# Kernel tuning notes

Hardware: AMD Instinct MI355X
Metric: run time of the kernel (lower is better)

Reference implementation:

```python
import jax, jax.numpy as jnp
import numpy as np

NEG_SLOPE = 0.2  # PyG GATConv default leaky_relu negative slope

N_NODES = 10000
N_EDGES = 80000
IN_FEAT = 200
HID = 400
IN_HEADS = 8
OUT_FEAT = 200


def setup_inputs() -> dict:
    key = jax.random.key(0)
    ks = jax.random.split(key, 12)
    input_data = jax.random.normal(ks[0], (N_NODES, IN_FEAT), dtype=jnp.float32)
    edge_index = jax.random.randint(ks[1], (2, N_EDGES), 0, N_NODES, dtype=jnp.int64)
    # conv1: GATConv(200 -> 400, heads=8, concat=True)
    W1 = jax.random.normal(ks[2], (IN_FEAT, IN_HEADS * HID), dtype=jnp.float32) * 0.05
    a_src1 = jax.random.normal(ks[3], (IN_HEADS, HID), dtype=jnp.float32) * 0.05
    a_dst1 = jax.random.normal(ks[4], (IN_HEADS, HID), dtype=jnp.float32) * 0.05
    b1 = jnp.zeros((IN_HEADS * HID,), dtype=jnp.float32)
    # conv2: GATConv(3200 -> 200, heads=1, concat=False)
    W2 = jax.random.normal(ks[5], (IN_HEADS * HID, 1 * OUT_FEAT), dtype=jnp.float32) * 0.05
    a_src2 = jax.random.normal(ks[6], (1, OUT_FEAT), dtype=jnp.float32) * 0.05
    a_dst2 = jax.random.normal(ks[7], (1, OUT_FEAT), dtype=jnp.float32) * 0.05
    b2 = jnp.zeros((OUT_FEAT,), dtype=jnp.float32)
    return {"input_data": input_data, "edge_index": edge_index,
            "W1": W1, "a_src1": a_src1, "a_dst1": a_dst1, "b1": b1,
            "W2": W2, "a_src2": a_src2, "a_dst2": a_dst2, "b2": b2}


def _gat_conv(x, src, dst, W, a_src, a_dst, b, heads, out_ch, concat):
    """PyG GATConv (v1 attention), eval mode (no dropout)."""
    n = x.shape[0]
    h = (x @ W).reshape(n, heads, out_ch)              # [N,H,C]
    al_s = jnp.sum(h * a_src, axis=-1)                 # [N,H]
    al_d = jnp.sum(h * a_dst, axis=-1)                 # [N,H]
    e = jax.nn.leaky_relu(al_s[src] + al_d[dst], NEG_SLOPE)  # [E,H]
    # segment softmax over edges sharing the same destination node
    e_max = jax.ops.segment_max(e, dst, num_segments=n)       # [N,H]
    e_exp = jnp.exp(e - e_max[dst])                            # [E,H]
    denom = jax.ops.segment_sum(e_exp, dst, num_segments=n)   # [N,H]
    alpha = e_exp / denom[dst]                                 # [E,H]
    msg = h[src] * alpha[:, :, None]                           # [E,H,C]
    out = jax.ops.segment_sum(msg, dst, num_segments=n)       # [N,H,C]
    out = out.reshape(n, heads * out_ch) if concat else out.mean(axis=1)
    return out + b


def reference(input_data, edge_index, W1, a_src1, a_dst1, b1, W2, a_src2, a_dst2, b2):
    n = input_data.shape[0]
    loop = jnp.arange(n, dtype=edge_index.dtype)
    src = jnp.concatenate([edge_index[0], loop])  # add self-loops (PyG default)
    dst = jnp.concatenate([edge_index[1], loop])
    # eval mode: F.dropout is identity
    x = _gat_conv(input_data, src, dst, W1, a_src1, a_dst1, b1, IN_HEADS, HID, True)
    x = jax.nn.elu(x)
    x = _gat_conv(x, src, dst, W2, a_src2, a_dst2, b2, 1, OUT_FEAT, False)
    return x
```

## Files before the change

kernel.cpp:

```cpp
#include <hip/hip_runtime.h>
#include <math.h>

#define N_NODES 10000
#define N_EDGES 80000
#define ET (N_EDGES + N_NODES)
#define IN_FEAT 200
#define HID 400
#define NH1 8
#define F1 (NH1 * HID)
#define OUT_FEAT 200
#define NEG_SLOPE 0.2f

#define M_PAD 10048
#define K1 224
#define HSL (NH1 * K1)
#define XH_K 416
#define C1P 448
#define KALL (NH1 * XH_K)
#define N2P2 256
#define XHS 456
#define NQ 4

typedef __attribute__((ext_vector_type(8))) short short8_t;
typedef __attribute__((ext_vector_type(4))) float f32x4;


__device__ inline void edge_sd(const int* __restrict__ ei, int e, int& s, int& d) {
    if (e < N_EDGES) { s = ei[e]; d = ei[N_EDGES + e]; }
    else { s = e - N_EDGES; d = s; }
}

__device__ inline unsigned short f2bf(float x) {
    unsigned u = __float_as_uint(x);
    unsigned r = u + 0x7FFFu + ((u >> 16) & 1u);
    return (unsigned short)(r >> 16);
}

__device__ inline void sm_merge(float& m, float& l, float m2, float l2) {
    float mn = fmaxf(m, m2);
    float t1 = (m  > -1e30f) ? l  * __expf(m  - mn) : 0.f;
    float t2 = (m2 > -1e30f) ? l2 * __expf(m2 - mn) : 0.f;
    m = mn; l = t1 + t2;
}

#define W1N (NH1 * C1P * K1)
#define W2N (N2P2 * KALL)
__global__ __launch_bounds__(256) void prep_w(const float* __restrict__ W1,
                                              const float* __restrict__ W2,
                                              unsigned short* __restrict__ W1f,
                                              unsigned short* __restrict__ W2f) {
    int idx = blockIdx.x * blockDim.x + threadIdx.x;
    if (idx < W1N) {
        int e    = idx & 7;
        int lane = (idx >> 3) & 63;
        int rem  = idx >> 9;
        int ks   = rem % 7;
        int jgh  = rem / 7;
        int jg   = jgh % 28;
        int h    = jgh / 28;
        int c = jg * 16 + (lane & 15);
        int k = ks * 32 + (lane >> 4) * 8 + e;
        float v = (k < IN_FEAT && c < HID) ? W1[(size_t)k * F1 + h * HID + c] : 0.f;
        W1f[idx] = f2bf(v);
    } else if (idx < W1N + W2N) {
        int t    = idx - W1N;
        int e    = t & 7;
        int lane = (t >> 3) & 63;
        int rem  = t >> 9;
        int ks   = rem % 13;
        int cgh  = rem / 13;
        int cg   = cgh % 16;
        int h    = cgh / 16;
        int c = cg * 16 + (lane & 15);
        int k = ks * 32 + (lane >> 4) * 8 + e;
        float v = (c < OUT_FEAT && k < HID) ? W2[(size_t)(h * HID + k) * OUT_FEAT + c] : 0.f;
        W2f[t] = f2bf(v);
    }
}

__global__ __launch_bounds__(256) void pvec_k(const float* __restrict__ W1,
                                              const float* __restrict__ a_src,
                                              const float* __restrict__ a_dst,
                                              float* __restrict__ p_src,
                                              float* __restrict__ p_dst) {
    int idx = blockIdx.x * blockDim.x + threadIdx.x;
    if (idx >= 2 * NH1 * IN_FEAT) return;
    int which = idx / (NH1 * IN_FEAT);
    int r = idx - which * (NH1 * IN_FEAT);
    int h = r / IN_FEAT, k = r - h * IN_FEAT;
    const float* av = (which == 0 ? a_src : a_dst) + h * HID;
    const float* wrow = W1 + (size_t)k * F1 + h * HID;
    float acc = 0.f;
    for (int c = 0; c < HID; ++c) acc += wrow[c] * av[c];
    (which == 0 ? p_src : p_dst)[h * IN_FEAT + k] = acc;
}

__global__ __launch_bounds__(512) void att1x(const float* __restrict__ X,
                                             const float* __restrict__ p_src,
                                             const float* __restrict__ p_dst,
                                             float* __restrict__ als,
                                             float* __restrict__ ald) {
    const int n    = blockIdx.x;
    const int head = threadIdx.x >> 6;
    const int lane = threadIdx.x & 63;
    const float* xp = X + (size_t)n * IN_FEAT;
    const float* ps = p_src + head * IN_FEAT;
    const float* pd = p_dst + head * IN_FEAT;
    float ss = 0.f, sd = 0.f;
    for (int k = lane; k < IN_FEAT; k += 64) {
        float v = xp[k];
        ss += v * ps[k];
        sd += v * pd[k];
    }
    for (int off = 32; off; off >>= 1) {
        ss += __shfl_down(ss, off);
        sd += __shfl_down(sd, off);
    }
    if (lane == 0) { als[n * NH1 + head] = ss; ald[n * NH1 + head] = sd; }
}

__global__ __launch_bounds__(256) void count_k(const int* __restrict__ ei, int* __restrict__ counts) {
    int e = blockIdx.x * blockDim.x + threadIdx.x;
    if (e >= ET) return;
    int s, d; edge_sd(ei, e, s, d);
    atomicAdd(&counts[d], 1);
}

__global__ __launch_bounds__(1024) void scan_k(const int* __restrict__ counts, int* __restrict__ offs) {
    __shared__ int part[1024];
    const int tid = threadIdx.x;
    const int base = tid * 10;
    int loc[10];
    int s = 0;
    for (int i = 0; i < 10; ++i) {
        int idx = base + i;
        int c = (idx < N_NODES) ? counts[idx] : 0;
        loc[i] = s; s += c;
    }
    part[tid] = s;
    __syncthreads();
    for (int off = 1; off < 1024; off <<= 1) {
        int v = (tid >= off) ? part[tid - off] : 0;
        __syncthreads();
        part[tid] += v;
        __syncthreads();
    }
    int pre = (tid > 0) ? part[tid - 1] : 0;
    for (int i = 0; i < 10; ++i) {
        int idx = base + i;
        if (idx < N_NODES) offs[idx] = pre + loc[i];
    }
    if (tid == 1023) offs[N_NODES] = part[1023];
}

__global__ __launch_bounds__(256) void scatter_k(const int* __restrict__ ei,
                                                 const int* __restrict__ offs,
                                                 int* __restrict__ cursor,
                                                 int* __restrict__ esrc) {
    int e = blockIdx.x * blockDim.x + threadIdx.x;
    if (e >= ET) return;
    int s, d; edge_sd(ei, e, s, d);
    int pos = atomicAdd(&cursor[d], 1);
    esrc[offs[d] + pos] = s;
}

__global__ __launch_bounds__(512) void agg1x(const float* __restrict__ X,
                                             const float* __restrict__ als1,
                                             const float* __restrict__ ald1,
                                             const int* __restrict__ offs,
                                             const int* __restrict__ esrc,
                                             unsigned short* __restrict__ xaggb) {
    __shared__ unsigned short sb[8][HSL];
    const int wave = threadIdx.x >> 6;
    const int lane = threadIdx.x & 63;
    const int n = blockIdx.x * 8 + wave;

    if (n < N_NODES) {
        float acc[NH1][4];
#pragma unroll
        for (int h = 0; h < NH1; ++h)
#pragma unroll
            for (int g = 0; g < 4; ++g) acc[h][g] = 0.f;

        const int beg = offs[n], end = offs[n + 1];
        const int grp = lane >> 3;
        const int hd  = lane & 7;
        const float aldv = ald1[n * NH1 + hd];

        float m = -INFINITY, l = 0.f;
        for (int t = beg + grp; t < end; t += 8) {
            const int s = esrc[t];
            float v = als1[s * NH1 + hd] + aldv;
            v = v > 0.f ? v : NEG_SLOPE * v;
            float mn = fmaxf(m, v);
            l = l * __expf(m - mn) + __expf(v - mn);
            m = mn;
        }
#pragma unroll
        for (int off = 8; off < 64; off <<= 1) {
            float m2 = __shfl_xor(m, off);
            float l2 = __shfl_xor(l, off);
            sm_merge(m, l, m2, l2);
        }
        const float inv_l = 1.f / l;

        for (int t = beg; t < end; ++t) {
            const int s = esrc[t];
            float aval = 0.f;
            if (lane < NH1) {
                float v = als1[s * NH1 + lane] + aldv;
                v = v > 0.f ? v : NEG_SLOPE * v;
                aval = __expf(v - m) * inv_l;
            }
            const float* xp = X + (size_t)s * IN_FEAT;
            float x0 = xp[lane];
            float x1 = xp[64 + lane];
            float x2 = xp[128 + lane];
            float x3 = (lane < 8) ? xp[192 + lane] : 0.f;
#pragma unroll
            for (int h = 0; h < NH1; ++h) {
                float a = __shfl(aval, h);
                acc[h][0] += a * x0;
                acc[h][1] += a * x1;
                acc[h][2] += a * x2;
                acc[h][3] += a * x3;
            }
        }
#pragma unroll
        for (int h = 0; h < NH1; ++h) {
            sb[wave][h * K1 + lane]        = f2bf(acc[h][0]);
            sb[wave][h * K1 + 64 + lane]   = f2bf(acc[h][1]);
            sb[wave][h * K1 + 128 + lane]  = f2bf(acc[h][2]);
            if (lane < 32) {
                unsigned short v3 = (lane < 8) ? f2bf(acc[h][3]) : (unsigned short)0;
                sb[wave][h * K1 + 192 + lane] = v3;
            }
        }
    } else {
        for (int j = lane; j < HSL; j += 64) sb[wave][j] = 0;
    }
    __syncthreads();
    const uint4* s4 = (const uint4*)(&sb[0][0]);
    uint4* d4 = (uint4*)(xaggb + (size_t)blockIdx.x * 8 * HSL);
    for (int c = threadIdx.x; c < 8 * HSL / 8; c += 512) d4[c] = s4[c];
}

__global__ __launch_bounds__(512, 2) void fused_gemm(const unsigned short* __restrict__ xaggb,
                                                     const unsigned short* __restrict__ W1f,
                                                     const float* __restrict__ b1,
                                                     const unsigned short* __restrict__ W2f,
                                                     float* __restrict__ h2p) {
    __shared__ unsigned short xhf[32 * XHS];
    const int wave = threadIdx.x >> 6;
    const int lane = threadIdx.x & 63;
    const int row  = lane & 15;
    const int kg   = lane >> 4;
    const int rg   = wave & 1;
    const int cg   = wave >> 1;
    const int m0   = blockIdx.x * 32 + rg * 16;
    const int c0   = cg * 112;
    const int c2   = cg * 64;

    f32x4 oacc[4];
#pragma unroll
    for (int j = 0; j < 4; ++j) oacc[j] = (f32x4){0.f, 0.f, 0.f, 0.f};

#pragma unroll
    for (int hh = 0; hh < 2; ++hh) {
        const int h = blockIdx.y * 2 + hh;
        if (hh > 0) __syncthreads();

        const unsigned short* ap = xaggb + (size_t)(m0 + row) * HSL + h * K1 + kg * 8;
        short8_t areg[7];
#pragma unroll
        for (int ks = 0; ks < 7; ++ks)
            areg[ks] = *(const short8_t*)(ap + ks * 32);

        const unsigned short* w1h = W1f + (((size_t)h * 28 + cg * 7) * 7) * 512 + lane * 8;
        f32x4 acc[7];
#pragma unroll
        for (int j = 0; j < 7; ++j) acc[j] = (f32x4){0.f, 0.f, 0.f, 0.f};
#pragma unroll
        for (int ks = 0; ks < 7; ++ks) {
            short8_t b[7];
#pragma unroll
            for (int j = 0; j < 7; ++j)
                b[j] = *(const short8_t*)(w1h + (size_t)(j * 7 + ks) * 512);
#pragma unroll
            for (int j = 0; j < 7; ++j)
                acc[j] = __builtin_amdgcn_mfma_f32_16x16x32_bf16(areg[ks], b[j], acc[j], 0, 0, 0);
        }

#pragma unroll
        for (int j = 0; j < 7; ++j) {
            int cc = c0 + j * 16 + row;
            float bias = (cc < HID) ? b1[h * HID + cc] : 0.f;
#pragma unroll
            for (int r = 0; r < 4; ++r) {
                int rl = rg * 16 + kg * 4 + r;
                float v = acc[j][r] + bias;
                v = v > 0.f ? v : (__expf(v) - 1.f);
                xhf[rl * XHS + cc] = f2bf(v);
            }
        }
        __syncthreads();

        const unsigned short* w2h = W2f + (((size_t)h * 16 + cg * 4) * 13) * 512 + lane * 8;
        const int rl = rg * 16 + row;
#pragma unroll
        for (int ks = 0; ks < 13; ++ks) {
            short8_t b[4];
#pragma unroll
            for (int j = 0; j < 4; ++j)
                b[j] = *(const short8_t*)(w2h + (size_t)(j * 13 + ks) * 512);
            short8_t a = *(const short8_t*)&xhf[rl * XHS + ks * 32 + kg * 8];
#pragma unroll
            for (int j = 0; j < 4; ++j)
                oacc[j] = __builtin_amdgcn_mfma_f32_16x16x32_bf16(a, b[j], oacc[j], 0, 0, 0);
        }
    }

    float* op = h2p + ((size_t)blockIdx.y * M_PAD + (m0 + kg * 4)) * OUT_FEAT;
#pragma unroll
    for (int j = 0; j < 4; ++j) {
        int cc = c2 + j * 16 + row;
        if (cc < OUT_FEAT) {
#pragma unroll
            for (int r = 0; r < 4; ++r)
                op[(size_t)r * OUT_FEAT + cc] = oacc[j][r];
        }
    }
}

__global__ __launch_bounds__(256) void reduce_att2(const float* __restrict__ h2p,
                                                   const float* __restrict__ a_src,
                                                   const float* __restrict__ a_dst,
                                                   float* __restrict__ h2,
                                                   float* __restrict__ als,
                                                   float* __restrict__ ald) {
    const int wave = threadIdx.x >> 6;
    const int lane = threadIdx.x & 63;
    const int row  = blockIdx.x * 4 + wave;

    f32x4 sum = {0.f, 0.f, 0.f, 0.f};
    if (lane < 50) {
        const float* p = h2p + (size_t)row * OUT_FEAT + lane * 4;
#pragma unroll
        for (int q = 0; q < NQ; ++q)
            sum += *(const f32x4*)(p + (size_t)q * M_PAD * OUT_FEAT);
        *(f32x4*)(h2 + (size_t)row * OUT_FEAT + lane * 4) = sum;
    }
    float ss = 0.f, sd = 0.f;
    if (lane < 50) {
        f32x4 as = *(const f32x4*)(a_src + lane * 4);
        f32x4 ad = *(const f32x4*)(a_dst + lane * 4);
#pragma unroll
        for (int j = 0; j < 4; ++j) { ss += sum[j] * as[j]; sd += sum[j] * ad[j]; }
    }
    for (int off = 32; off; off >>= 1) {
        ss += __shfl_down(ss, off);
        sd += __shfl_down(sd, off);
    }
    if (lane == 0 && row < N_NODES) { als[row] = ss; ald[row] = sd; }
}

__global__ __launch_bounds__(256) void agg2_csr(const float* __restrict__ h2,
                                                const float* __restrict__ als2,
                                                const float* __restrict__ ald2,
                                                const int* __restrict__ offs,
                                                const int* __restrict__ esrc,
                                                const float* __restrict__ b2,
                                                float* __restrict__ out) {
    __shared__ float sm, sl;
    const int n = blockIdx.x;
    const int k = threadIdx.x;
    const float aldn = ald2[n];
    const int beg = offs[n], end = offs[n + 1];

    if (k < 64) {
        float m = -INFINITY, l = 0.f;
        for (int t = beg + k; t < end; t += 64) {
            int s = esrc[t];
            float v = als2[s] + aldn;
            v = v > 0.f ? v : NEG_SLOPE * v;
            float mn = fmaxf(m, v);
            l = l * __expf(m - mn) + __expf(v - mn);
            m = mn;
        }
#pragma unroll
        for (int off = 1; off < 64; off <<= 1) {
            float m2 = __shfl_xor(m, off);
            float l2 = __shfl_xor(l, off);
            sm_merge(m, l, m2, l2);
        }
        if (k == 0) { sm = m; sl = 1.f / l; }
    }
    __syncthreads();
    const float m = sm, inv_l = sl;

    if (k >= OUT_FEAT) return;
    float acc = 0.f;
    for (int t = beg; t < end; ++t) {
        int s = esrc[t];
        float v = als2[s] + aldn;
        v = v > 0.f ? v : NEG_SLOPE * v;
        float a = __expf(v - m) * inv_l;
        acc += a * h2[(size_t)s * OUT_FEAT + k];
    }
    out[(size_t)n * OUT_FEAT + k] = acc + b2[k];
}

extern "C" void kernel_launch(void* const* d_in, const int* in_sizes, int n_in,
                              void* d_out, int out_size, void* d_ws, size_t ws_size,
                              hipStream_t stream) {
    const float* X   = (const float*)d_in[0];
    const int*   ei  = (const int*)d_in[1];
    const float* W1  = (const float*)d_in[2];
    const float* as1 = (const float*)d_in[3];
    const float* ad1 = (const float*)d_in[4];
    const float* b1  = (const float*)d_in[5];
    const float* W2  = (const float*)d_in[6];
    const float* as2 = (const float*)d_in[7];
    const float* ad2 = (const float*)d_in[8];
    const float* b2  = (const float*)d_in[9];
    float* out = (float*)d_out;

    char* base = (char*)d_ws;
    auto carve = [&](size_t bytes) -> void* {
        void* p = (void*)base;
        base += (bytes + 255) & ~(size_t)255;
        return p;
    };
    float* p_src1 = (float*)carve(NH1 * IN_FEAT * 4);
    float* p_dst1 = (float*)carve(NH1 * IN_FEAT * 4);
    float* als1   = (float*)carve(N_NODES * NH1 * 4);
    float* ald1   = (float*)carve(N_NODES * NH1 * 4);
    float* als2   = (float*)carve(N_NODES * 4);
    float* ald2   = (float*)carve(N_NODES * 4);
    float* h2     = (float*)carve((size_t)M_PAD * OUT_FEAT * 4);
    int* counts   = (int*)carve(N_NODES * 4);
    int* cursor   = (int*)carve(N_NODES * 4);
    int* offs     = (int*)carve((N_NODES + 1) * 4);
    int* esrc     = (int*)carve(ET * 4);
    unsigned short* xaggb = (unsigned short*)carve((size_t)M_PAD * HSL * 2);
    unsigned short* W1f   = (unsigned short*)carve((size_t)W1N * 2);
    unsigned short* W2f   = (unsigned short*)carve((size_t)W2N * 2);
    float* h2p    = (float*)carve((size_t)NQ * M_PAD * OUT_FEAT * 4);

    hipMemsetAsync(counts, 0, 2 * 40192, stream);

    count_k<<<(ET + 255) / 256, 256, 0, stream>>>(ei, counts);
    scan_k<<<1, 1024, 0, stream>>>(counts, offs);
    scatter_k<<<(ET + 255) / 256, 256, 0, stream>>>(ei, offs, cursor, esrc);
    prep_w<<<(W1N + W2N + 255) / 256, 256, 0, stream>>>(W1, W2, W1f, W2f);
    pvec_k<<<(2 * NH1 * IN_FEAT + 255) / 256, 256, 0, stream>>>(W1, as1, ad1, p_src1, p_dst1);
    att1x<<<N_NODES, 512, 0, stream>>>(X, p_src1, p_dst1, als1, ald1);

    agg1x<<<M_PAD / 8, 512, 0, stream>>>(X, als1, ald1, offs, esrc, xaggb);

    fused_gemm<<<dim3(M_PAD / 32, NQ), 512, 0, stream>>>(xaggb, W1f, b1, W2f, h2p);

    reduce_att2<<<M_PAD / 4, 256, 0, stream>>>(h2p, as2, ad2, h2, als2, ald2);

    agg2_csr<<<N_NODES, 256, 0, stream>>>(h2, als2, ald2, offs, esrc, b2, out);
}
```

Baseline: 235.7 us.

## Merge preprocessing kernels and store aggregated features in MFMA fragment layout

Weight prep, edge counting and attention-vector projection now run as one launch, and the scatter runs together with the layer-1 attention logits in a second launch. This cuts the number of kernel launches and lets independent work overlap inside each launch. The aggregation kernel also writes its bf16 output directly in the 16-row MFMA A-fragment tile order, so the fused GEMM loads each fragment with contiguous per-lane reads instead of strided row reads. In exchange, the agg1x store becomes a scattered 16-byte write pattern, and the merged kernels run with block sizes that do not suit every branch.

Measured after the change: 218.7 us, median of 2. -7.2%, faster.

```diff
diff --git a/kernel.cpp b/kernel.cpp
--- a/kernel.cpp
+++ b/kernel.cpp
@@ -45,85 +45,67 @@
 
 #define W1N (NH1 * C1P * K1)
 #define W2N (N2P2 * KALL)
-__global__ __launch_bounds__(256) void prep_w(const float* __restrict__ W1,
-                                              const float* __restrict__ W2,
-                                              unsigned short* __restrict__ W1f,
-                                              unsigned short* __restrict__ W2f) {
-    int idx = blockIdx.x * blockDim.x + threadIdx.x;
-    if (idx < W1N) {
-        int e    = idx & 7;
-        int lane = (idx >> 3) & 63;
-        int rem  = idx >> 9;
-        int ks   = rem % 7;
-        int jgh  = rem / 7;
-        int jg   = jgh % 28;
-        int h    = jgh / 28;
-        int c = jg * 16 + (lane & 15);
-        int k = ks * 32 + (lane >> 4) * 8 + e;
-        float v = (k < IN_FEAT && c < HID) ? W1[(size_t)k * F1 + h * HID + c] : 0.f;
-        W1f[idx] = f2bf(v);
-    } else if (idx < W1N + W2N) {
-        int t    = idx - W1N;
-        int e    = t & 7;
-        int lane = (t >> 3) & 63;
-        int rem  = t >> 9;
-        int ks   = rem % 13;
-        int cgh  = rem / 13;
-        int cg   = cgh % 16;
-        int h    = cgh / 16;
-        int c = cg * 16 + (lane & 15);
-        int k = ks * 32 + (lane >> 4) * 8 + e;
-        float v = (c < OUT_FEAT && k < HID) ? W2[(size_t)(h * HID + k) * OUT_FEAT + c] : 0.f;
-        W2f[t] = f2bf(v);
-    }
-}
-
-__global__ __launch_bounds__(256) void pvec_k(const float* __restrict__ W1,
-                                              const float* __restrict__ a_src,
-                                              const float* __restrict__ a_dst,
-                                              float* __restrict__ p_src,
-                                              float* __restrict__ p_dst) {
-    int idx = blockIdx.x * blockDim.x + threadIdx.x;
-    if (idx >= 2 * NH1 * IN_FEAT) return;
-    int which = idx / (NH1 * IN_FEAT);
-    int r = idx - which * (NH1 * IN_FEAT);
-    int h = r / IN_FEAT, k = r - h * IN_FEAT;
-    const float* av = (which == 0 ? a_src : a_dst) + h * HID;
-    const float* wrow = W1 + (size_t)k * F1 + h * HID;
-    float acc = 0.f;
-    for (int c = 0; c < HID; ++c) acc += wrow[c] * av[c];
-    (which == 0 ? p_src : p_dst)[h * IN_FEAT + k] = acc;
-}
-
-__global__ __launch_bounds__(512) void att1x(const float* __restrict__ X,
-                                             const float* __restrict__ p_src,
-                                             const float* __restrict__ p_dst,
-                                             float* __restrict__ als,
-                                             float* __restrict__ ald) {
-    const int n    = blockIdx.x;
-    const int head = threadIdx.x >> 6;
-    const int lane = threadIdx.x & 63;
-    const float* xp = X + (size_t)n * IN_FEAT;
-    const float* ps = p_src + head * IN_FEAT;
-    const float* pd = p_dst + head * IN_FEAT;
-    float ss = 0.f, sd = 0.f;
-    for (int k = lane; k < IN_FEAT; k += 64) {
-        float v = xp[k];
-        ss += v * ps[k];
-        sd += v * pd[k];
-    }
-    for (int off = 32; off; off >>= 1) {
-        ss += __shfl_down(ss, off);
-        sd += __shfl_down(sd, off);
-    }
-    if (lane == 0) { als[n * NH1 + head] = ss; ald[n * NH1 + head] = sd; }
-}
-
-__global__ __launch_bounds__(256) void count_k(const int* __restrict__ ei, int* __restrict__ counts) {
-    int e = blockIdx.x * blockDim.x + threadIdx.x;
-    if (e >= ET) return;
-    int s, d; edge_sd(ei, e, s, d);
-    atomicAdd(&counts[d], 1);
+#define PW_BLK ((W1N + W2N + 255) / 256)
+#define CNT_BLK ((ET + 255) / 256)
+#define PV_BLK ((2 * NH1 * IN_FEAT + 255) / 256)
+__global__ __launch_bounds__(256) void pre_k(const float* __restrict__ W1,
+                                             const float* __restrict__ W2,
+                                             const int* __restrict__ ei,
+                                             const float* __restrict__ a_src,
+                                             const float* __restrict__ a_dst,
+                                             unsigned short* __restrict__ W1f,
+                                             unsigned short* __restrict__ W2f,
+                                             int* __restrict__ counts,
+                                             float* __restrict__ p_src,
+                                             float* __restrict__ p_dst) {
+    const int bid = blockIdx.x;
+    if (bid < PW_BLK) {
+        int idx = bid * 256 + threadIdx.x;
+        if (idx < W1N) {
+            int e    = idx & 7;
+            int lane = (idx >> 3) & 63;
+            int rem  = idx >> 9;
+            int ks   = rem % 7;
+            int jgh  = rem / 7;
+            int jg   = jgh % 28;
+            int h    = jgh / 28;
+            int c = jg * 16 + (lane & 15);
+            int k = ks * 32 + (lane >> 4) * 8 + e;
+            float v = (k < IN_FEAT && c < HID) ? W1[(size_t)k * F1 + h * HID + c] : 0.f;
+            W1f[idx] = f2bf(v);
+        } else if (idx < W1N + W2N) {
+            int t    = idx - W1N;
+            int e    = t & 7;
+            int lane = (t >> 3) & 63;
+            int rem  = t >> 9;
+            int ks   = rem % 13;
+            int cgh  = rem / 13;
+            int cg   = cgh % 16;
+            int h    = cgh / 16;
+            int c = cg * 16 + (lane & 15);
+            int k = ks * 32 + (lane >> 4) * 8 + e;
+            float v = (c < OUT_FEAT && k < HID) ? W2[(size_t)(h * HID + k) * OUT_FEAT + c] : 0.f;
+            W2f[t] = f2bf(v);
+        }
+    } else if (bid < PW_BLK + CNT_BLK) {
+        int e = (bid - PW_BLK) * 256 + threadIdx.x;
+        if (e < ET) {
+            int s, d; edge_sd(ei, e, s, d);
+            atomicAdd(&counts[d], 1);
+        }
+    } else {
+        int idx = (bid - PW_BLK - CNT_BLK) * 256 + threadIdx.x;
+        if (idx < 2 * NH1 * IN_FEAT) {
+            int which = idx / (NH1 * IN_FEAT);
+            int r = idx - which * (NH1 * IN_FEAT);
+            int h = r / IN_FEAT, k = r - h * IN_FEAT;
+            const float* av = (which == 0 ? a_src : a_dst) + h * HID;
+            const float* wrow = W1 + (size_t)k * F1 + h * HID;
+            float acc = 0.f;
+            for (int c = 0; c < HID; ++c) acc += wrow[c] * av[c];
+            (which == 0 ? p_src : p_dst)[h * IN_FEAT + k] = acc;
+        }
+    }
 }
 
 __global__ __launch_bounds__(1024) void scan_k(const int* __restrict__ counts, int* __restrict__ offs) {
@@ -153,15 +135,43 @@
     if (tid == 1023) offs[N_NODES] = part[1023];
 }
 
-__global__ __launch_bounds__(256) void scatter_k(const int* __restrict__ ei,
-                                                 const int* __restrict__ offs,
-                                                 int* __restrict__ cursor,
-                                                 int* __restrict__ esrc) {
-    int e = blockIdx.x * blockDim.x + threadIdx.x;
-    if (e >= ET) return;
-    int s, d; edge_sd(ei, e, s, d);
-    int pos = atomicAdd(&cursor[d], 1);
-    esrc[offs[d] + pos] = s;
+#define SC_BLK ((ET + 511) / 512)
+__global__ __launch_bounds__(512) void mid_k(const int* __restrict__ ei,
+                                             const int* __restrict__ offs,
+                                             int* __restrict__ cursor,
+                                             int* __restrict__ esrc,
+                                             const float* __restrict__ X,
+                                             const float* __restrict__ p_src,
+                                             const float* __restrict__ p_dst,
+                                             float* __restrict__ als,
+                                             float* __restrict__ ald) {
+    const int bid = blockIdx.x;
+    if (bid < SC_BLK) {
+        int e = bid * 512 + threadIdx.x;
+        if (e < ET) {
+            int s, d; edge_sd(ei, e, s, d);
+            int pos = atomicAdd(&cursor[d], 1);
+            esrc[offs[d] + pos] = s;
+        }
+    } else {
+        const int n    = bid - SC_BLK;
+        const int head = threadIdx.x >> 6;
+        const int lane = threadIdx.x & 63;
+        const float* xp = X + (size_t)n * IN_FEAT;
+        const float* ps = p_src + head * IN_FEAT;
+        const float* pd = p_dst + head * IN_FEAT;
+        float ss = 0.f, sd = 0.f;
+        for (int k = lane; k < IN_FEAT; k += 64) {
+            float v = xp[k];
+            ss += v * ps[k];
+            sd += v * pd[k];
+        }
+        for (int off = 32; off; off >>= 1) {
+            ss += __shfl_down(ss, off);
+            sd += __shfl_down(sd, off);
+        }
+        if (lane == 0) { als[n * NH1 + head] = ss; ald[n * NH1 + head] = sd; }
+    }
 }
 
 __global__ __launch_bounds__(512) void agg1x(const float* __restrict__ X,
@@ -240,9 +250,20 @@
         for (int j = lane; j < HSL; j += 64) sb[wave][j] = 0;
     }
     __syncthreads();
-    const uint4* s4 = (const uint4*)(&sb[0][0]);
-    uint4* d4 = (uint4*)(xaggb + (size_t)blockIdx.x * 8 * HSL);
-    for (int c = threadIdx.x; c < 8 * HSL / 8; c += 512) d4[c] = s4[c];
+
+    const int mtile = blockIdx.x >> 1;
+    const int half8 = (blockIdx.x & 1) * 8;
+    for (int q = threadIdx.x; q < 1792; q += 512) {
+        const int i  = q & 7;
+        const int kg = (q >> 3) & 3;
+        const int r2 = q >> 5;
+        const int ks = r2 % 7;
+        const int h  = r2 / 7;
+        const uint4* s = (const uint4*)&sb[i][h * K1 + ks * 32 + kg * 8];
+        uint4* d = (uint4*)(xaggb + (((size_t)mtile * NH1 + h) * 7 + ks) * 512
+                                  + (size_t)(kg * 16 + half8 + i) * 8);
+        *d = *s;
+    }
 }
 
 __global__ __launch_bounds__(512, 2) void fused_gemm(const unsigned short* __restrict__ xaggb,
@@ -257,7 +278,8 @@
     const int kg   = lane >> 4;
     const int rg   = wave & 1;
     const int cg   = wave >> 1;
-    const int m0   = blockIdx.x * 32 + rg * 16;
+    const int mtile = blockIdx.x * 2 + rg;
+    const int m0    = mtile * 16;
     const int c0   = cg * 112;
     const int c2   = cg * 64;
 
@@ -270,11 +292,11 @@
         const int h = blockIdx.y * 2 + hh;
         if (hh > 0) __syncthreads();
 
-        const unsigned short* ap = xaggb + (size_t)(m0 + row) * HSL + h * K1 + kg * 8;
+        const unsigned short* ap = xaggb + (((size_t)mtile * NH1 + h) * 7) * 512 + lane * 8;
         short8_t areg[7];
 #pragma unroll
         for (int ks = 0; ks < 7; ++ks)
-            areg[ks] = *(const short8_t*)(ap + ks * 32);
+            areg[ks] = *(const short8_t*)(ap + ks * 512);
 
         const unsigned short* w1h = W1f + (((size_t)h * 28 + cg * 7) * 7) * 512 + lane * 8;
         f32x4 acc[7];
@@ -442,19 +464,18 @@
     int* cursor   = (int*)carve(N_NODES * 4);
     int* offs     = (int*)carve((N_NODES + 1) * 4);
     int* esrc     = (int*)carve(ET * 4);
-    unsigned short* xaggb = (unsigned short*)carve((size_t)M_PAD * HSL * 2);
+    unsigned short* xaggb = (unsigned short*)carve((size_t)(M_PAD / 16) * NH1 * 7 * 512 * 2);
     unsigned short* W1f   = (unsigned short*)carve((size_t)W1N * 2);
     unsigned short* W2f   = (unsigned short*)carve((size_t)W2N * 2);
     float* h2p    = (float*)carve((size_t)NQ * M_PAD * OUT_FEAT * 4);
 
     hipMemsetAsync(counts, 0, 2 * 40192, stream);
 
-    count_k<<<(ET + 255) / 256, 256, 0, stream>>>(ei, counts);
+    pre_k<<<PW_BLK + CNT_BLK + PV_BLK, 256, 0, stream>>>(W1, W2, ei, as1, ad1,
+                                                         W1f, W2f, counts, p_src1, p_dst1);
     scan_k<<<1, 1024, 0, stream>>>(counts, offs);
-    scatter_k<<<(ET + 255) / 256, 256, 0, stream>>>(ei, offs, cursor, esrc);
-    prep_w<<<(W1N + W2N + 255) / 256, 256, 0, stream>>>(W1, W2, W1f, W2f);
-    pvec_k<<<(2 * NH1 * IN_FEAT + 255) / 256, 256, 0, stream>>>(W1, as1, ad1, p_src1, p_dst1);
-    att1x<<<N_NODES, 512, 0, stream>>>(X, p_src1, p_dst1, als1, ald1);
+    mid_k<<<SC_BLK + N_NODES, 512, 0, stream>>>(ei, offs, cursor, esrc,
+                                                X, p_src1, p_dst1, als1, ald1);
 
     agg1x<<<M_PAD / 8, 512, 0, stream>>>(X, als1, ald1, offs, esrc, xaggb);
 
```
